# Performance work log

Measured on AMD Instinct MI355X. Metric: run time of the kernel, lower is better.

Reference implementation:

```python
import jax, jax.numpy as jnp
import numpy as np

HIDDEN_DIM = 2048
CODE_DIM = 256
CODEBOOK_SIZE = 512
FC_DIMS = [1024, 512]
BATCH = 16384
EPS = 1e-5
NEG_SLOPE = 0.01  # PyTorch LeakyReLU default


def _linear_init(key, fan_in, fan_out):
    # kaiming_uniform_(a=sqrt(3)) ~= U(-1/sqrt(fan_in), 1/sqrt(fan_in)) scaled; use uniform bound
    bound = 1.0 / np.sqrt(fan_in)
    return jax.random.uniform(key, (fan_in, fan_out), jnp.float32, -bound, bound)


def setup_inputs() -> dict:
    key = jax.random.key(0)
    ks = jax.random.split(key, 16)
    h = jax.random.normal(ks[0], (BATCH, HIDDEN_DIM), jnp.float32)
    # encoder: Linear(2048->1024, no bias), BN, LReLU, Linear(1024->512, no bias), BN, LReLU, Linear(512->256, bias)
    enc_w1 = _linear_init(ks[1], HIDDEN_DIM, FC_DIMS[0])
    enc_bn1_g = jnp.ones((FC_DIMS[0],), jnp.float32)
    enc_bn1_b = jnp.zeros((FC_DIMS[0],), jnp.float32)
    enc_w2 = _linear_init(ks[2], FC_DIMS[0], FC_DIMS[1])
    enc_bn2_g = jnp.ones((FC_DIMS[1],), jnp.float32)
    enc_bn2_b = jnp.zeros((FC_DIMS[1],), jnp.float32)
    enc_w3 = _linear_init(ks[3], FC_DIMS[1], CODE_DIM)
    enc_b3 = jax.random.uniform(ks[4], (CODE_DIM,), jnp.float32, -1/np.sqrt(FC_DIMS[1]), 1/np.sqrt(FC_DIMS[1]))
    # codebook: NearestEmbed weight shape (code_dim, codebook_size)
    codebook = jax.random.normal(ks[5], (CODE_DIM, CODEBOOK_SIZE), jnp.float32)
    # decoder: Linear(256->512, no bias), BN, LReLU, Linear(512->1024, no bias), BN, LReLU, Linear(1024->2048, bias)
    dec_w1 = _linear_init(ks[6], CODE_DIM, FC_DIMS[1])
    dec_bn1_g = jnp.ones((FC_DIMS[1],), jnp.float32)
    dec_bn1_b = jnp.zeros((FC_DIMS[1],), jnp.float32)
    dec_w2 = _linear_init(ks[7], FC_DIMS[1], FC_DIMS[0])
    dec_bn2_g = jnp.ones((FC_DIMS[0],), jnp.float32)
    dec_bn2_b = jnp.zeros((FC_DIMS[0],), jnp.float32)
    dec_w3 = _linear_init(ks[8], FC_DIMS[0], HIDDEN_DIM)
    dec_b3 = jax.random.uniform(ks[9], (HIDDEN_DIM,), jnp.float32, -1/np.sqrt(FC_DIMS[0]), 1/np.sqrt(FC_DIMS[0]))
    return dict(h=h, enc_w1=enc_w1, enc_bn1_g=enc_bn1_g, enc_bn1_b=enc_bn1_b,
                enc_w2=enc_w2, enc_bn2_g=enc_bn2_g, enc_bn2_b=enc_bn2_b,
                enc_w3=enc_w3, enc_b3=enc_b3, codebook=codebook,
                dec_w1=dec_w1, dec_bn1_g=dec_bn1_g, dec_bn1_b=dec_bn1_b,
                dec_w2=dec_w2, dec_bn2_g=dec_bn2_g, dec_bn2_b=dec_bn2_b,
                dec_w3=dec_w3, dec_b3=dec_b3)


def _bn(x, g, b):
    # BatchNorm1d, training mode: biased batch variance, eps=1e-5
    mu = jnp.mean(x, axis=0)
    var = jnp.var(x, axis=0)
    return (x - mu) * jax.lax.rsqrt(var + EPS) * g + b


def _lrelu(x):
    return jnp.where(x >= 0, x, NEG_SLOPE * x)


def _quantize(z_e, codebook):
    # nearest codebook entry; codebook is [code_dim, K]
    # dist[b,k] = ||z_e[b] - codebook[:,k]||^2 (expanded, drop constant ||z||^2 for argmin? keep full for clarity)
    d = (jnp.sum(z_e * z_e, axis=1, keepdims=True)
         - 2.0 * (z_e @ codebook)
         + jnp.sum(codebook * codebook, axis=0)[None, :])  # [B, K]
    idx = jnp.argmin(d, axis=1)  # [B]
    z_q = codebook.T[idx]        # [B, code_dim]
    return z_q, idx


def reference(h, enc_w1, enc_bn1_g, enc_bn1_b, enc_w2, enc_bn2_g, enc_bn2_b,
              enc_w3, enc_b3, codebook,
              dec_w1, dec_bn1_g, dec_bn1_b, dec_w2, dec_bn2_g, dec_bn2_b,
              dec_w3, dec_b3):
    # encoder
    x = _lrelu(_bn(h @ enc_w1, enc_bn1_g, enc_bn1_b))
    x = _lrelu(_bn(x @ enc_w2, enc_bn2_g, enc_bn2_b))
    z_e = x @ enc_w3 + enc_b3  # [B, code_dim]
    # nearest-embed quantization with straight-through estimator
    z_q_raw, code_indices = _quantize(z_e, codebook)
    z_q = z_e + jax.lax.stop_gradient(z_q_raw - z_e)
    # decoder
    y = _lrelu(_bn(z_q @ dec_w1, dec_bn1_g, dec_bn1_b))
    y = _lrelu(_bn(y @ dec_w2, dec_bn2_g, dec_bn2_b))
    h_recon = y @ dec_w3 + dec_b3  # [B, hidden_dim]
    return z_e, z_q, h_recon, code_indices
```

## Files before the change

kernel.cpp:

```cpp
#include <hip/hip_runtime.h>
#include <hip/hip_fp16.h>
#include <cstdint>
#include <cstddef>

typedef _Float16 f16;
typedef _Float16 half8 __attribute__((ext_vector_type(8)));
typedef _Float16 half4 __attribute__((ext_vector_type(4)));
typedef float floatx4 __attribute__((ext_vector_type(4)));

static constexpr size_t NB  = 16384;
static constexpr size_t DH  = 2048;
static constexpr size_t F1  = 1024;
static constexpr size_t F2  = 512;
static constexpr size_t CD  = 256;
static constexpr size_t KCB = 512;

static constexpr size_t ZE_OFF  = 0;
static constexpr size_t ZQ_OFF  = NB * CD;
static constexpr size_t HR_OFF  = 2 * NB * CD;
static constexpr size_t IDX_OFF = 2 * NB * CD + NB * DH;

static constexpr size_t O_HH   = 0;
static constexpr size_t O_HL   = O_HH + NB * DH * 2;
static constexpr size_t R1_END = O_HL + NB * DH * 2;

static constexpr size_t R_X1H = 0;
static constexpr size_t R_X1L = NB * F1 * 2;
static constexpr size_t R_X2F = 2 * NB * F1 * 2;
static constexpr size_t R_X2H = R_X2F + NB * F2 * 4;
static constexpr size_t R_X2L = R_X2H + NB * F2 * 2;
static constexpr size_t R_Y1F = 0;
static constexpr size_t R_Y1H = NB * F2 * 4;
static constexpr size_t R_Y2H = 0;

static constexpr size_t O_W1H = R1_END;
static constexpr size_t O_W1L = O_W1H + F1 * DH * 2;
static constexpr size_t O_W2H = O_W1L + F1 * DH * 2;
static constexpr size_t O_W2L = O_W2H + F2 * F1 * 2;
static constexpr size_t O_W3H = O_W2L + F2 * F1 * 2;
static constexpr size_t O_W3L = O_W3H + CD * F2 * 2;
static constexpr size_t O_CBH = O_W3L + CD * F2 * 2;
static constexpr size_t O_CBL = O_CBH + KCB * CD * 2;
static constexpr size_t O_DW1 = O_CBL + KCB * CD * 2;
static constexpr size_t O_DW2 = O_DW1 + F2 * CD * 2;
static constexpr size_t O_DW3 = O_DW2 + F1 * F2 * 2;
static constexpr size_t O_SUM = O_DW3 + DH * F1 * 2;
static constexpr size_t O_SQ  = O_SUM + 4 * 1024 * 8;
static constexpr size_t O_SC  = O_SQ + 4 * 1024 * 8;
static constexpr size_t O_SH  = O_SC + 4 * 1024 * 4;
static constexpr size_t O_CN  = O_SH + 4 * 1024 * 4;
static constexpr size_t R2    = (O_CN + 4096 + 255) & ~(size_t)255;
static constexpr size_t R2_X1F = R2;
static constexpr size_t R2_ZEH = R2;
static constexpr size_t R2_ZEL = R2 + NB * CD * 2;
static constexpr size_t R2_S   = R2 + 2 * NB * CD * 2;
static constexpr size_t R2_ZQH = R2_S + NB * KCB * 4;
static constexpr size_t R2_Y2F = R2;

#define GLLDS(src, dst)                                                          \
    __builtin_amdgcn_global_load_lds(                                            \
        (const __attribute__((address_space(1))) void*)(src),                    \
        (__attribute__((address_space(3))) void*)(dst), 16, 0, 0)

#define VMCNT(n)  asm volatile("s_waitcnt vmcnt(" #n ")" ::: "memory")

#define WAITC(n) do { switch (n) {                                               \
    case 0: asm volatile("s_waitcnt lgkmcnt(0)" ::: "memory"); break;            \
    case 1: asm volatile("s_waitcnt lgkmcnt(1)" ::: "memory"); break;            \
    case 2: asm volatile("s_waitcnt lgkmcnt(2)" ::: "memory"); break;            \
    case 3: asm volatile("s_waitcnt lgkmcnt(3)" ::: "memory"); break;            \
    case 4: asm volatile("s_waitcnt lgkmcnt(4)" ::: "memory"); break;            \
    case 5: asm volatile("s_waitcnt lgkmcnt(5)" ::: "memory"); break;            \
    case 6: asm volatile("s_waitcnt lgkmcnt(6)" ::: "memory"); break;            \
    default: asm volatile("s_waitcnt lgkmcnt(7)" ::: "memory"); break; }         \
    __builtin_amdgcn_sched_barrier(0); } while (0)

template<bool BIAS, bool STATS, bool WSPLIT>
__global__ __launch_bounds__(256)
void g3s(const f16* __restrict__ Ah_, const f16* __restrict__ Al_,
         const f16* __restrict__ Bh_, const f16* __restrict__ Bl_,
         float* __restrict__ C, const float* __restrict__ bias,
         double* __restrict__ ssum, double* __restrict__ ssq,
         f16* __restrict__ zeh, f16* __restrict__ zel,
         int M, int N, int K)
{
    __shared__ f16 lds[2][2][8192];
    const int tid  = threadIdx.x;
    const int lane = tid & 63;
    const int w    = tid >> 6;
    const int wr   = w >> 1, wn = w & 1;
    const int row0 = blockIdx.x * 128;
    const int col0 = blockIdx.y * 128;

    const int rr8 = lane >> 3;
    const int p   = (lane & 7) ^ rr8;
    const int rr  = w * 32 + rr8;
    const f16* srcH = (p < 4) ? (Ah_ + (size_t)(row0 + rr) * K + p * 8)
                              : (Bh_ + (size_t)(col0 + rr) * K + (p - 4) * 8);
    const f16* srcL = (p < 4) ? (Al_ + (size_t)(row0 + rr) * K + p * 8)
                              : (Bl_ + (size_t)(col0 + rr) * K + (p - 4) * 8);
    const int dstBase = w * 32 * 64;
    const int KT = K >> 5;

    floatx4 acc[4][4];
#pragma unroll
    for (int m = 0; m < 4; ++m)
#pragma unroll
        for (int n = 0; n < 4; ++n)
#pragma unroll
            for (int j = 0; j < 4; ++j) acc[m][n][j] = 0.f;

    const int l15 = lane & 15;
    const int sA  = lane >> 4;

    int rdA[4], rdB[4];
#pragma unroll
    for (int m = 0; m < 4; ++m) {
        const int rA = wr * 64 + m * 16 + l15;
        rdA[m] = rA * 64 + ((sA ^ (rA & 7)) << 3);
    }
#pragma unroll
    for (int n = 0; n < 4; ++n) {
        const int rB = wn * 64 + n * 16 + l15;
        rdB[n] = rB * 64 + (((4 + sA) ^ (rB & 7)) << 3);
    }

#pragma unroll
    for (int j = 0; j < 4; ++j)
        GLLDS(srcH + (size_t)j * 8 * K, &lds[0][0][dstBase + j * 512]);
#pragma unroll
    for (int j = 0; j < 4; ++j)
        GLLDS(srcL + (size_t)j * 8 * K, &lds[0][1][dstBase + j * 512]);
    VMCNT(4);
    __builtin_amdgcn_s_barrier();

    half8 afh[4], afl[4], bfh[4], bfl[4];

    for (int kt = 0; kt < KT; ++kt) {
        const int cur = kt & 1, nxt = cur ^ 1;
        const int koff = (kt + 1 < KT ? kt + 1 : kt) << 5;
        const f16* plH = lds[cur][0];
        const f16* plL = lds[cur][1];

#pragma unroll
        for (int n = 0; n < 4; ++n) bfh[n] = *(const half8*)(plH + rdB[n]);
        afh[0] = *(const half8*)(plH + rdA[0]);
        afh[1] = *(const half8*)(plH + rdA[1]);
#pragma unroll
        for (int j = 0; j < 4; ++j)
            GLLDS(srcH + (size_t)j * 8 * K + koff, &lds[nxt][0][dstBase + j * 512]);
        WAITC(1);
        __builtin_amdgcn_s_setprio(1);
#pragma unroll
        for (int m = 0; m < 4; ++m) {
            if (m + 2 < 4) afh[m + 2] = *(const half8*)(plH + rdA[m + 2]);
#pragma unroll
            for (int n = 0; n < 4; ++n)
                acc[m][n] = __builtin_amdgcn_mfma_f32_16x16x32_f16(afh[m], bfh[n], acc[m][n], 0, 0, 0);
            if (m + 1 < 4) { if (m + 2 < 4) WAITC(1); else WAITC(0); }
        }
        __builtin_amdgcn_s_setprio(0);
        VMCNT(4);
        __builtin_amdgcn_s_barrier();

#pragma unroll
        for (int n = 0; n < 4; ++n) bfl[n] = *(const half8*)(plL + rdB[n]);
        afl[0] = *(const half8*)(plL + rdA[0]);
        afl[1] = *(const half8*)(plL + rdA[1]);
#pragma unroll
        for (int j = 0; j < 4; ++j)
            GLLDS(srcL + (size_t)j * 8 * K + koff, &lds[nxt][1][dstBase + j * 512]);
        WAITC(2);
        __builtin_amdgcn_s_setprio(1);
#pragma unroll
        for (int m = 0; m < 4; ++m) {
            if (m + 2 < 4) afl[m + 2] = *(const half8*)(plL + rdA[m + 2]);
#pragma unroll
            for (int n = 0; n < 4; ++n)
                acc[m][n] = __builtin_amdgcn_mfma_f32_16x16x32_f16(afh[m], bfl[n], acc[m][n], 0, 0, 0);
        }
#pragma unroll
        for (int m = 0; m < 4; ++m) {
            WAITC(3 - m);
#pragma unroll
            for (int n = 0; n < 4; ++n)
                acc[m][n] = __builtin_amdgcn_mfma_f32_16x16x32_f16(afl[m], bfh[n], acc[m][n], 0, 0, 0);
        }
        __builtin_amdgcn_s_setprio(0);
        VMCNT(4);
        __builtin_amdgcn_s_barrier();
    }
    VMCNT(0);

    const int cb0 = col0 + wn * 64;
    const int rb0 = row0 + wr * 64 + (lane >> 4) * 4;
#pragma unroll
    for (int n = 0; n < 4; ++n) {
        const int col = cb0 + n * 16 + l15;
        const float bv = BIAS ? bias[col] : 0.f;
        double sd = 0.0, sq = 0.0;
#pragma unroll
        for (int m = 0; m < 4; ++m) {
            const int row = rb0 + m * 16;
#pragma unroll
            for (int j = 0; j < 4; ++j) {
                const float v = acc[m][n][j] + bv;
                const size_t o = (size_t)(row + j) * N + col;
                C[o] = v;
                if (WSPLIT) {
                    const f16 hv = (f16)v;
                    zeh[o] = hv;
                    zel[o] = (f16)(v - (float)hv);
                }
                if (STATS) { sd += (double)v; sq += (double)v * (double)v; }
            }
        }
        if (STATS) {
            sd += __shfl_xor(sd, 16);
            sd += __shfl_xor(sd, 32);
            sq += __shfl_xor(sq, 16);
            sq += __shfl_xor(sq, 32);
            if (lane < 16) {
                atomicAdd(ssum + col, sd);
                atomicAdd(ssq + col, sq);
            }
        }
    }
}

template<bool BIAS, bool STATS>
__global__ __launch_bounds__(256)
void g1s(const f16* __restrict__ A_, const f16* __restrict__ B_,
         float* __restrict__ C, const float* __restrict__ bias,
         double* __restrict__ ssum, double* __restrict__ ssq,
         int M, int N, int K)
{
    __shared__ f16 lds[3][8192];
    const int tid  = threadIdx.x;
    const int lane = tid & 63;
    const int w    = tid >> 6;
    const int wr   = w >> 1, wn = w & 1;
    const int row0 = blockIdx.x * 128;
    const int col0 = blockIdx.y * 128;

    const int rr8 = lane >> 3;
    const int p   = (lane & 7) ^ rr8;
    const int rr  = w * 32 + rr8;
    const f16* srcH = (p < 4) ? (A_ + (size_t)(row0 + rr) * K + p * 8)
                              : (B_ + (size_t)(col0 + rr) * K + (p - 4) * 8);
    const int dstBase = w * 32 * 64;
    const int KT = K >> 5;

    floatx4 acc[4][4];
#pragma unroll
    for (int m = 0; m < 4; ++m)
#pragma unroll
        for (int n = 0; n < 4; ++n)
#pragma unroll
            for (int j = 0; j < 4; ++j) acc[m][n][j] = 0.f;

    const int l15 = lane & 15;
    const int sA  = lane >> 4;

    int rdA[4], rdB[4];
#pragma unroll
    for (int m = 0; m < 4; ++m) {
        const int rA = wr * 64 + m * 16 + l15;
        rdA[m] = rA * 64 + ((sA ^ (rA & 7)) << 3);
    }
#pragma unroll
    for (int n = 0; n < 4; ++n) {
        const int rB = wn * 64 + n * 16 + l15;
        rdB[n] = rB * 64 + (((4 + sA) ^ (rB & 7)) << 3);
    }

#pragma unroll
    for (int j = 0; j < 4; ++j)
        GLLDS(srcH + (size_t)j * 8 * K, &lds[0][dstBase + j * 512]);
    {
        const int k1 = (KT > 1 ? 1 : 0) << 5;
#pragma unroll
        for (int j = 0; j < 4; ++j)
            GLLDS(srcH + (size_t)j * 8 * K + k1, &lds[1][dstBase + j * 512]);
    }
    VMCNT(4);
    __builtin_amdgcn_s_barrier();

    half8 afh[4], bfh[4];

    for (int kt = 0; kt < KT; ++kt) {
        const int cur = kt % 3, tgt = (kt + 2) % 3;
        const int koff = (kt + 2 < KT ? kt + 2 : KT - 1) << 5;
        const f16* plH = lds[cur];

#pragma unroll
        for (int n = 0; n < 4; ++n) bfh[n] = *(const half8*)(plH + rdB[n]);
        afh[0] = *(const half8*)(plH + rdA[0]);
        afh[1] = *(const half8*)(plH + rdA[1]);
#pragma unroll
        for (int j = 0; j < 4; ++j)
            GLLDS(srcH + (size_t)j * 8 * K + koff, &lds[tgt][dstBase + j * 512]);
        WAITC(1);
        __builtin_amdgcn_s_setprio(1);
#pragma unroll
        for (int m = 0; m < 4; ++m) {
            if (m + 2 < 4) afh[m + 2] = *(const half8*)(plH + rdA[m + 2]);
#pragma unroll
            for (int n = 0; n < 4; ++n)
                acc[m][n] = __builtin_amdgcn_mfma_f32_16x16x32_f16(afh[m], bfh[n], acc[m][n], 0, 0, 0);
            if (m + 1 < 4) { if (m + 2 < 4) WAITC(1); else WAITC(0); }
        }
        __builtin_amdgcn_s_setprio(0);
        VMCNT(4);
        __builtin_amdgcn_s_barrier();
    }
    VMCNT(0);

    const int cb0 = col0 + wn * 64;
    const int rb0 = row0 + wr * 64 + (lane >> 4) * 4;
#pragma unroll
    for (int n = 0; n < 4; ++n) {
        const int col = cb0 + n * 16 + l15;
        const float bv = BIAS ? bias[col] : 0.f;
        double sd = 0.0, sq = 0.0;
#pragma unroll
        for (int m = 0; m < 4; ++m) {
            const int row = rb0 + m * 16;
#pragma unroll
            for (int j = 0; j < 4; ++j) {
                const float v = acc[m][n][j] + bv;
                C[(size_t)(row + j) * N + col] = v;
                if (STATS) { sd += (double)v; sq += (double)v * (double)v; }
            }
        }
        if (STATS) {
            sd += __shfl_xor(sd, 16);
            sd += __shfl_xor(sd, 32);
            sq += __shfl_xor(sq, 16);
            sq += __shfl_xor(sq, 32);
            if (lane < 16) {
                atomicAdd(ssum + col, sd);
                atomicAdd(ssq + col, sq);
            }
        }
    }
}

__global__ void split_f32(const float* __restrict__ X, f16* __restrict__ hi,
                          f16* __restrict__ lo, size_t n4)
{
    const size_t stride = (size_t)gridDim.x * blockDim.x;
    for (size_t i = (size_t)blockIdx.x * blockDim.x + threadIdx.x; i < n4; i += stride) {
        const floatx4 x = ((const floatx4*)X)[i];
        half4 h, l;
#pragma unroll
        for (int j = 0; j < 4; ++j) {
            const float v = x[j];
            const f16 hv = (f16)v;
            h[j] = hv;
            l[j] = (f16)(v - (float)hv);
        }
        ((half4*)hi)[i] = h;
        ((half4*)lo)[i] = l;
    }
}

template<bool SPLIT>
__global__ void bn_apply(const float* __restrict__ X, const float* __restrict__ scale,
                         const float* __restrict__ shift, f16* __restrict__ Yhi,
                         f16* __restrict__ Ylo, size_t n4, int Nmask)
{
    const size_t stride = (size_t)gridDim.x * blockDim.x;
    for (size_t i = (size_t)blockIdx.x * blockDim.x + threadIdx.x; i < n4; i += stride) {
        const floatx4 x = ((const floatx4*)X)[i];
        const int col = (int)((i * 4) & (size_t)Nmask);
        half4 h, l;
#pragma unroll
        for (int j = 0; j < 4; ++j) {
            float v = x[j] * scale[col + j] + shift[col + j];
            v = v >= 0.f ? v : 0.01f * v;
            const f16 hv = (f16)v;
            h[j] = hv;
            if (SPLIT) l[j] = (f16)(v - (float)hv);
        }
        ((half4*)Yhi)[i] = h;
        if (SPLIT) ((half4*)Ylo)[i] = l;
    }
}

__global__ void bn_finalize(const double* __restrict__ ssum, const double* __restrict__ ssq,
                            const float* __restrict__ g, const float* __restrict__ b,
                            float* __restrict__ scale, float* __restrict__ shift, int N)
{
    const int j = blockIdx.x * blockDim.x + threadIdx.x;
    if (j < N) {
        const double inv = 1.0 / (double)NB;
        const double mean = ssum[j] * inv;
        const double var  = ssq[j] * inv - mean * mean;
        const double sc   = (double)g[j] / sqrt(var + 1e-5);
        scale[j] = (float)sc;
        shift[j] = (float)((double)b[j] - mean * sc);
    }
}

__device__ __forceinline__ void tr_body(const float* __restrict__ W, f16* __restrict__ Thi,
                                        f16* __restrict__ Tlo, int K, int N,
                                        int bx, int by, bool split)
{
    __shared__ float tile[32][33];
    const int x = threadIdx.x;
    const int y = threadIdx.y;
    const int nt = bx * 32;
    const int kt = by * 32;
#pragma unroll
    for (int i = 0; i < 32; i += 8)
        tile[y + i][x] = W[(size_t)(kt + y + i) * N + nt + x];
    __syncthreads();
#pragma unroll
    for (int i = 0; i < 32; i += 8) {
        const float v = tile[x][y + i];
        const size_t o = (size_t)(nt + y + i) * K + kt + x;
        const f16 hv = (f16)v;
        Thi[o] = hv;
        if (split) Tlo[o] = (f16)(v - (float)hv);
    }
}

__global__ void prep_weights(const float* __restrict__ ew1, const float* __restrict__ ew2,
                             const float* __restrict__ ew3, const float* __restrict__ cbk,
                             const float* __restrict__ dw1, const float* __restrict__ dw2,
                             const float* __restrict__ dw3,
                             f16* __restrict__ W1h, f16* __restrict__ W1l,
                             f16* __restrict__ W2h, f16* __restrict__ W2l,
                             f16* __restrict__ W3h, f16* __restrict__ W3l,
                             f16* __restrict__ CBh, f16* __restrict__ CBl,
                             f16* __restrict__ D1t, f16* __restrict__ D2t,
                             f16* __restrict__ D3t, float* __restrict__ cn)
{
    const int b = blockIdx.x;
    if (b < 2048)      tr_body(ew1, W1h, W1l, DH, F1, b % 32, b / 32, true);
    else if (b < 2560) { const int c = b - 2048; tr_body(ew2, W2h, W2l, F1, F2, c % 16, c / 16, true); }
    else if (b < 2688) { const int c = b - 2560; tr_body(ew3, W3h, W3l, F2, CD, c % 8,  c / 8,  true); }
    else if (b < 2816) { const int c = b - 2688; tr_body(cbk, CBh, CBl, CD, KCB, c % 16, c / 16, true); }
    else if (b < 2944) { const int c = b - 2816; tr_body(dw1, D1t, nullptr, CD, F2, c % 16, c / 16, false); }
    else if (b < 3456) { const int c = b - 2944; tr_body(dw2, D2t, nullptr, F2, F1, c % 32, c / 32, false); }
    else if (b < 5504) { const int c = b - 3456; tr_body(dw3, D3t, nullptr, F1, DH, c % 64, c / 64, false); }
    else {
        const int tid = threadIdx.y * 32 + threadIdx.x;
        const int k = (b - 5504) * 256 + tid;
        if (k < (int)KCB) {
            double s = 0.0;
            for (int d = 0; d < (int)CD; ++d) {
                const float v = cbk[(size_t)d * KCB + k];
                s += (double)v * v;
            }
            cn[k] = (float)s;
        }
    }
}

__global__ void argmin_gather(const float* __restrict__ S, const float* __restrict__ cn,
                              const float* __restrict__ cb, float* __restrict__ zq,
                              float* __restrict__ idx_out, f16* __restrict__ zqh)
{
    const int lane = threadIdx.x & 63;
    const int row  = blockIdx.x * 4 + (threadIdx.x >> 6);
    const float* Sr = S + (size_t)row * KCB;
    float best = 3.4e38f;
    int bi = 0;
#pragma unroll
    for (int i = 0; i < 8; ++i) {
        const int k = lane + 64 * i;
        const float d = cn[k] - 2.f * Sr[k];
        if (d < best) { best = d; bi = k; }
    }
#pragma unroll
    for (int off = 32; off > 0; off >>= 1) {
        const float ob = __shfl_xor(best, off);
        const int   oi = __shfl_xor(bi, off);
        if (ob < best || (ob == best && oi < bi)) { best = ob; bi = oi; }
    }
    if (lane == 0) idx_out[row] = (float)bi;
#pragma unroll
    for (int i = 0; i < 4; ++i) {
        const int d = lane + 64 * i;
        const float v = cb[(size_t)d * KCB + bi];
        zq[(size_t)row * CD + d]  = v;
        zqh[(size_t)row * CD + d] = (f16)v;
    }
}

extern "C" void kernel_launch(void* const* d_in, const int* in_sizes, int n_in,
                              void* d_out, int out_size, void* d_ws, size_t ws_size,
                              hipStream_t stream)
{
    (void)in_sizes; (void)n_in; (void)out_size; (void)ws_size;
    const float* h   = (const float*)d_in[0];
    const float* ew1 = (const float*)d_in[1];
    const float* bg1 = (const float*)d_in[2];
    const float* bb1 = (const float*)d_in[3];
    const float* ew2 = (const float*)d_in[4];
    const float* bg2 = (const float*)d_in[5];
    const float* bb2 = (const float*)d_in[6];
    const float* ew3 = (const float*)d_in[7];
    const float* eb3 = (const float*)d_in[8];
    const float* cb  = (const float*)d_in[9];
    const float* dw1 = (const float*)d_in[10];
    const float* dg1 = (const float*)d_in[11];
    const float* db1 = (const float*)d_in[12];
    const float* dw2 = (const float*)d_in[13];
    const float* dg2 = (const float*)d_in[14];
    const float* db2 = (const float*)d_in[15];
    const float* dw3 = (const float*)d_in[16];
    const float* db3 = (const float*)d_in[17];

    char* ws = (char*)d_ws;
    float* out = (float*)d_out;

    f16* Hh  = (f16*)(ws + O_HH);
    f16* Hl  = (f16*)(ws + O_HL);
    f16* W1h = (f16*)(ws + O_W1H);
    f16* W1l = (f16*)(ws + O_W1L);
    f16* W2h = (f16*)(ws + O_W2H);
    f16* W2l = (f16*)(ws + O_W2L);
    f16* W3h = (f16*)(ws + O_W3H);
    f16* W3l = (f16*)(ws + O_W3L);
    f16* CBh = (f16*)(ws + O_CBH);
    f16* CBl = (f16*)(ws + O_CBL);
    f16* D1t = (f16*)(ws + O_DW1);
    f16* D2t = (f16*)(ws + O_DW2);
    f16* D3t = (f16*)(ws + O_DW3);
    double* sum0 = (double*)(ws + O_SUM);
    double* sq0  = (double*)(ws + O_SQ);
    float* sc0 = (float*)(ws + O_SC);
    float* sh0 = (float*)(ws + O_SH);
    float* cn  = (float*)(ws + O_CN);

    float* X1f = (float*)(ws + R2_X1F);
    f16*  X1h = (f16*)(ws + R_X1H);
    f16*  X1l = (f16*)(ws + R_X1L);
    float* X2f = (float*)(ws + R_X2F);
    f16*  X2h = (f16*)(ws + R_X2H);
    f16*  X2l = (f16*)(ws + R_X2L);
    f16*  Zeh = (f16*)(ws + R2_ZEH);
    f16*  Zel = (f16*)(ws + R2_ZEL);
    float* Sb  = (float*)(ws + R2_S);
    f16*  Zqh = (f16*)(ws + R2_ZQH);
    float* Y1f = (float*)(ws + R_Y1F);
    f16*  Y1h = (f16*)(ws + R_Y1H);
    float* Y2f = (float*)(ws + R2_Y2F);
    f16*  Y2h = (f16*)(ws + R_Y2H);

    hipMemsetAsync(ws + O_SUM, 0, 4 * 1024 * 8 * 2, stream);

    split_f32<<<2048, 256, 0, stream>>>(h, Hh, Hl, NB * DH / 4);
    prep_weights<<<5506, dim3(32, 8), 0, stream>>>(ew1, ew2, ew3, cb, dw1, dw2, dw3,
        W1h, W1l, W2h, W2l, W3h, W3l, CBh, CBl, D1t, D2t, D3t, cn);

    g3s<false, true, false><<<dim3(NB / 128, F1 / 128), 256, 0, stream>>>(
        Hh, Hl, W1h, W1l, X1f, nullptr, sum0, sq0, nullptr, nullptr, NB, F1, DH);
    bn_finalize<<<4, 256, 0, stream>>>(sum0, sq0, bg1, bb1, sc0, sh0, F1);
    bn_apply<true><<<2048, 256, 0, stream>>>(X1f, sc0, sh0, X1h, X1l, NB * F1 / 4, (int)F1 - 1);

    g3s<false, true, false><<<dim3(NB / 128, F2 / 128), 256, 0, stream>>>(
        X1h, X1l, W2h, W2l, X2f, nullptr, sum0 + 1024, sq0 + 1024, nullptr, nullptr, NB, F2, F1);
    bn_finalize<<<2, 256, 0, stream>>>(sum0 + 1024, sq0 + 1024, bg2, bb2, sc0 + 1024, sh0 + 1024, F2);
    bn_apply<true><<<2048, 256, 0, stream>>>(X2f, sc0 + 1024, sh0 + 1024, X2h, X2l, NB * F2 / 4, (int)F2 - 1);

    g3s<true, false, true><<<dim3(NB / 128, CD / 128), 256, 0, stream>>>(
        X2h, X2l, W3h, W3l, out + ZE_OFF, eb3, nullptr, nullptr, Zeh, Zel, NB, CD, F2);

    g3s<false, false, false><<<dim3(NB / 128, KCB / 128), 256, 0, stream>>>(
        Zeh, Zel, CBh, CBl, Sb, nullptr, nullptr, nullptr, nullptr, nullptr, NB, KCB, CD);
    argmin_gather<<<NB / 4, 256, 0, stream>>>(Sb, cn, cb, out + ZQ_OFF, out + IDX_OFF, Zqh);

    g1s<false, true><<<dim3(NB / 128, F2 / 128), 256, 0, stream>>>(
        Zqh, D1t, Y1f, nullptr, sum0 + 2048, sq0 + 2048, NB, F2, CD);
    bn_finalize<<<2, 256, 0, stream>>>(sum0 + 2048, sq0 + 2048, dg1, db1, sc0 + 2048, sh0 + 2048, F2);
    bn_apply<false><<<2048, 256, 0, stream>>>(Y1f, sc0 + 2048, sh0 + 2048, Y1h, nullptr, NB * F2 / 4, (int)F2 - 1);

    g1s<false, true><<<dim3(NB / 128, F1 / 128), 256, 0, stream>>>(
        Y1h, D2t, Y2f, nullptr, sum0 + 3072, sq0 + 3072, NB, F1, F2);
    bn_finalize<<<4, 256, 0, stream>>>(sum0 + 3072, sq0 + 3072, dg2, db2, sc0 + 3072, sh0 + 3072, F1);
    bn_apply<false><<<2048, 256, 0, stream>>>(Y2f, sc0 + 3072, sh0 + 3072, Y2h, nullptr, NB * F1 / 4, (int)F1 - 1);

    g1s<true, false><<<dim3(NB / 128, DH / 128), 256, 0, stream>>>(
        Y2h, D3t, out + HR_OFF, db3, nullptr, nullptr, NB, DH, F1);
}
```

Measured before the change: 667.2 us.

## Enlarge GEMM tiles to 256-wide with 512 threads and 32x32x16 MFMA

```diff
diff --git a/kernel.cpp b/kernel.cpp
--- a/kernel.cpp
+++ b/kernel.cpp
@@ -7,6 +7,7 @@
 typedef _Float16 half8 __attribute__((ext_vector_type(8)));
 typedef _Float16 half4 __attribute__((ext_vector_type(4)));
 typedef float floatx4 __attribute__((ext_vector_type(4)));
+typedef float floatx16 __attribute__((ext_vector_type(16)));
 
 static constexpr size_t NB  = 16384;
 static constexpr size_t DH  = 2048;
@@ -63,66 +64,63 @@
         (__attribute__((address_space(3))) void*)(dst), 16, 0, 0)
 
 #define VMCNT(n)  asm volatile("s_waitcnt vmcnt(" #n ")" ::: "memory")
-
-#define WAITC(n) do { switch (n) {                                               \
-    case 0: asm volatile("s_waitcnt lgkmcnt(0)" ::: "memory"); break;            \
-    case 1: asm volatile("s_waitcnt lgkmcnt(1)" ::: "memory"); break;            \
-    case 2: asm volatile("s_waitcnt lgkmcnt(2)" ::: "memory"); break;            \
-    case 3: asm volatile("s_waitcnt lgkmcnt(3)" ::: "memory"); break;            \
-    case 4: asm volatile("s_waitcnt lgkmcnt(4)" ::: "memory"); break;            \
-    case 5: asm volatile("s_waitcnt lgkmcnt(5)" ::: "memory"); break;            \
-    case 6: asm volatile("s_waitcnt lgkmcnt(6)" ::: "memory"); break;            \
-    default: asm volatile("s_waitcnt lgkmcnt(7)" ::: "memory"); break; }         \
+#define LGKMCNT0 do { asm volatile("s_waitcnt lgkmcnt(0)" ::: "memory");         \
     __builtin_amdgcn_sched_barrier(0); } while (0)
 
-template<bool BIAS, bool STATS, bool WSPLIT>
-__global__ __launch_bounds__(256)
-void g3s(const f16* __restrict__ Ah_, const f16* __restrict__ Al_,
-         const f16* __restrict__ Bh_, const f16* __restrict__ Bl_,
-         float* __restrict__ C, const float* __restrict__ bias,
-         double* __restrict__ ssum, double* __restrict__ ssq,
-         f16* __restrict__ zeh, f16* __restrict__ zel,
-         int M, int N, int K)
-{
-    __shared__ f16 lds[2][2][8192];
+template<int MB, bool BIAS, bool STATS, bool WSPLIT>
+__global__ __launch_bounds__(512)
+void gemm3_w(const f16* __restrict__ Ah_, const f16* __restrict__ Al_,
+             const f16* __restrict__ Bh_, const f16* __restrict__ Bl_,
+             float* __restrict__ C, const float* __restrict__ bias,
+             double* __restrict__ ssum, double* __restrict__ ssq,
+             f16* __restrict__ zeh, f16* __restrict__ zel,
+             int M, int N, int K)
+{
+    constexpr int BM = MB * 64;
+    __shared__ f16 lds[2][2][16384];
     const int tid  = threadIdx.x;
     const int lane = tid & 63;
     const int w    = tid >> 6;
-    const int wr   = w >> 1, wn = w & 1;
-    const int row0 = blockIdx.x * 128;
-    const int col0 = blockIdx.y * 128;
+    const int wr   = w >> 2, wn = w & 3;
+    const int row0 = blockIdx.x * BM;
+    const int col0 = blockIdx.y * 256;
 
     const int rr8 = lane >> 3;
     const int p   = (lane & 7) ^ rr8;
     const int rr  = w * 32 + rr8;
-    const f16* srcH = (p < 4) ? (Ah_ + (size_t)(row0 + rr) * K + p * 8)
+    const int arr = rr & (BM - 1);
+    const f16* srcH = (p < 4) ? (Ah_ + (size_t)(row0 + arr) * K + p * 8)
                               : (Bh_ + (size_t)(col0 + rr) * K + (p - 4) * 8);
-    const f16* srcL = (p < 4) ? (Al_ + (size_t)(row0 + rr) * K + p * 8)
+    const f16* srcL = (p < 4) ? (Al_ + (size_t)(row0 + arr) * K + p * 8)
                               : (Bl_ + (size_t)(col0 + rr) * K + (p - 4) * 8);
     const int dstBase = w * 32 * 64;
     const int KT = K >> 5;
 
-    floatx4 acc[4][4];
-#pragma unroll
-    for (int m = 0; m < 4; ++m)
-#pragma unroll
-        for (int n = 0; n < 4; ++n)
-#pragma unroll
-            for (int j = 0; j < 4; ++j) acc[m][n][j] = 0.f;
-
-    const int l15 = lane & 15;
-    const int sA  = lane >> 4;
-
-    int rdA[4], rdB[4];
-#pragma unroll
-    for (int m = 0; m < 4; ++m) {
-        const int rA = wr * 64 + m * 16 + l15;
-        rdA[m] = rA * 64 + ((sA ^ (rA & 7)) << 3);
-    }
-#pragma unroll
-    for (int n = 0; n < 4; ++n) {
-        const int rB = wn * 64 + n * 16 + l15;
-        rdB[n] = rB * 64 + (((4 + sA) ^ (rB & 7)) << 3);
+    floatx16 acc[MB][2];
+#pragma unroll
+    for (int bm = 0; bm < MB; ++bm)
+#pragma unroll
+        for (int bn = 0; bn < 2; ++bn)
+#pragma unroll
+            for (int j = 0; j < 16; ++j) acc[bm][bn][j] = 0.f;
+
+    const int l31  = lane & 31;
+    const int hsel = lane >> 5;
+
+    int rdA[MB][2], rdB[2][2];
+#pragma unroll
+    for (int bm = 0; bm < MB; ++bm) {
+        const int rA = wr * (MB * 32) + bm * 32 + l31;
+#pragma unroll
+        for (int t = 0; t < 2; ++t)
+            rdA[bm][t] = rA * 64 + (((hsel + 2 * t) ^ (rA & 7)) << 3);
+    }
+#pragma unroll
+    for (int bn = 0; bn < 2; ++bn) {
+        const int rB = wn * 64 + bn * 32 + l31;
+#pragma unroll
+        for (int t = 0; t < 2; ++t)
+            rdB[bn][t] = rB * 64 + (((4 + hsel + 2 * t) ^ (rB & 7)) << 3);
     }
 
 #pragma unroll
@@ -134,7 +132,7 @@
     VMCNT(4);
     __builtin_amdgcn_s_barrier();
 
-    half8 afh[4], afl[4], bfh[4], bfl[4];
+    half8 afh[MB][2], afl[MB][2], bfh[2][2], bfl[2][2];
 
     for (int kt = 0; kt < KT; ++kt) {
         const int cur = kt & 1, nxt = cur ^ 1;
@@ -143,69 +141,79 @@
         const f16* plL = lds[cur][1];
 
 #pragma unroll
-        for (int n = 0; n < 4; ++n) bfh[n] = *(const half8*)(plH + rdB[n]);
-        afh[0] = *(const half8*)(plH + rdA[0]);
-        afh[1] = *(const half8*)(plH + rdA[1]);
+        for (int bn = 0; bn < 2; ++bn)
+#pragma unroll
+            for (int t = 0; t < 2; ++t)
+                bfh[bn][t] = *(const half8*)(plH + rdB[bn][t]);
+#pragma unroll
+        for (int bm = 0; bm < MB; ++bm)
+#pragma unroll
+            for (int t = 0; t < 2; ++t)
+                afh[bm][t] = *(const half8*)(plH + rdA[bm][t]);
 #pragma unroll
         for (int j = 0; j < 4; ++j)
             GLLDS(srcH + (size_t)j * 8 * K + koff, &lds[nxt][0][dstBase + j * 512]);
-        WAITC(1);
+        LGKMCNT0;
         __builtin_amdgcn_s_setprio(1);
 #pragma unroll
-        for (int m = 0; m < 4; ++m) {
-            if (m + 2 < 4) afh[m + 2] = *(const half8*)(plH + rdA[m + 2]);
-#pragma unroll
-            for (int n = 0; n < 4; ++n)
-                acc[m][n] = __builtin_amdgcn_mfma_f32_16x16x32_f16(afh[m], bfh[n], acc[m][n], 0, 0, 0);
-            if (m + 1 < 4) { if (m + 2 < 4) WAITC(1); else WAITC(0); }
-        }
+        for (int bm = 0; bm < MB; ++bm)
+#pragma unroll
+            for (int bn = 0; bn < 2; ++bn) {
+                acc[bm][bn] = __builtin_amdgcn_mfma_f32_32x32x16_f16(afh[bm][0], bfh[bn][0], acc[bm][bn], 0, 0, 0);
+                acc[bm][bn] = __builtin_amdgcn_mfma_f32_32x32x16_f16(afh[bm][1], bfh[bn][1], acc[bm][bn], 0, 0, 0);
+            }
         __builtin_amdgcn_s_setprio(0);
         VMCNT(4);
         __builtin_amdgcn_s_barrier();
 
 #pragma unroll
-        for (int n = 0; n < 4; ++n) bfl[n] = *(const half8*)(plL + rdB[n]);
-        afl[0] = *(const half8*)(plL + rdA[0]);
-        afl[1] = *(const half8*)(plL + rdA[1]);
+        for (int bn = 0; bn < 2; ++bn)
+#pragma unroll
+            for (int t = 0; t < 2; ++t)
+                bfl[bn][t] = *(const half8*)(plL + rdB[bn][t]);
+#pragma unroll
+        for (int bm = 0; bm < MB; ++bm)
+#pragma unroll
+            for (int t = 0; t < 2; ++t)
+                afl[bm][t] = *(const half8*)(plL + rdA[bm][t]);
 #pragma unroll
         for (int j = 0; j < 4; ++j)
             GLLDS(srcL + (size_t)j * 8 * K + koff, &lds[nxt][1][dstBase + j * 512]);
-        WAITC(2);
+        LGKMCNT0;
         __builtin_amdgcn_s_setprio(1);
 #pragma unroll
-        for (int m = 0; m < 4; ++m) {
-            if (m + 2 < 4) afl[m + 2] = *(const half8*)(plL + rdA[m + 2]);
-#pragma unroll
-            for (int n = 0; n < 4; ++n)
-                acc[m][n] = __builtin_amdgcn_mfma_f32_16x16x32_f16(afh[m], bfl[n], acc[m][n], 0, 0, 0);
-        }
-#pragma unroll
-        for (int m = 0; m < 4; ++m) {
-            WAITC(3 - m);
-#pragma unroll
-            for (int n = 0; n < 4; ++n)
-                acc[m][n] = __builtin_amdgcn_mfma_f32_16x16x32_f16(afl[m], bfh[n], acc[m][n], 0, 0, 0);
-        }
+        for (int bm = 0; bm < MB; ++bm)
+#pragma unroll
+            for (int bn = 0; bn < 2; ++bn) {
+                acc[bm][bn] = __builtin_amdgcn_mfma_f32_32x32x16_f16(afh[bm][0], bfl[bn][0], acc[bm][bn], 0, 0, 0);
+                acc[bm][bn] = __builtin_amdgcn_mfma_f32_32x32x16_f16(afh[bm][1], bfl[bn][1], acc[bm][bn], 0, 0, 0);
+            }
+#pragma unroll
+        for (int bm = 0; bm < MB; ++bm)
+#pragma unroll
+            for (int bn = 0; bn < 2; ++bn) {
+                acc[bm][bn] = __builtin_amdgcn_mfma_f32_32x32x16_f16(afl[bm][0], bfh[bn][0], acc[bm][bn], 0, 0, 0);
+                acc[bm][bn] = __builtin_amdgcn_mfma_f32_32x32x16_f16(afl[bm][1], bfh[bn][1], acc[bm][bn], 0, 0, 0);
+            }
         __builtin_amdgcn_s_setprio(0);
         VMCNT(4);
         __builtin_amdgcn_s_barrier();
     }
     VMCNT(0);
 
-    const int cb0 = col0 + wn * 64;
-    const int rb0 = row0 + wr * 64 + (lane >> 4) * 4;
-#pragma unroll
-    for (int n = 0; n < 4; ++n) {
-        const int col = cb0 + n * 16 + l15;
+#pragma unroll
+    for (int bn = 0; bn < 2; ++bn) {
+        const int col = col0 + wn * 64 + bn * 32 + l31;
         const float bv = BIAS ? bias[col] : 0.f;
         double sd = 0.0, sq = 0.0;
 #pragma unroll
-        for (int m = 0; m < 4; ++m) {
-            const int row = rb0 + m * 16;
-#pragma unroll
-            for (int j = 0; j < 4; ++j) {
-                const float v = acc[m][n][j] + bv;
-                const size_t o = (size_t)(row + j) * N + col;
+        for (int bm = 0; bm < MB; ++bm) {
+            const int rb = row0 + wr * (MB * 32) + bm * 32 + 4 * hsel;
+#pragma unroll
+            for (int r = 0; r < 16; ++r) {
+                const int row = rb + (r & 3) + 8 * (r >> 2);
+                const float v = acc[bm][bn][r] + bv;
+                const size_t o = (size_t)row * N + col;
                 C[o] = v;
                 if (WSPLIT) {
                     const f16 hv = (f16)v;
@@ -216,11 +224,9 @@
             }
         }
         if (STATS) {
-            sd += __shfl_xor(sd, 16);
             sd += __shfl_xor(sd, 32);
-            sq += __shfl_xor(sq, 16);
             sq += __shfl_xor(sq, 32);
-            if (lane < 16) {
+            if (lane < 32) {
                 atomicAdd(ssum + col, sd);
                 atomicAdd(ssq + col, sq);
             }
@@ -228,50 +234,56 @@
     }
 }
 
-template<bool BIAS, bool STATS>
-__global__ __launch_bounds__(256)
-void g1s(const f16* __restrict__ A_, const f16* __restrict__ B_,
-         float* __restrict__ C, const float* __restrict__ bias,
-         double* __restrict__ ssum, double* __restrict__ ssq,
-         int M, int N, int K)
-{
-    __shared__ f16 lds[3][8192];
+template<int MB, bool BIAS, bool STATS>
+__global__ __launch_bounds__(512)
+void gemm1_w(const f16* __restrict__ A_, const f16* __restrict__ B_,
+             float* __restrict__ C, const float* __restrict__ bias,
+             double* __restrict__ ssum, double* __restrict__ ssq,
+             int M, int N, int K)
+{
+    constexpr int BM = MB * 64;
+    __shared__ f16 lds[3][16384];
     const int tid  = threadIdx.x;
     const int lane = tid & 63;
     const int w    = tid >> 6;
-    const int wr   = w >> 1, wn = w & 1;
-    const int row0 = blockIdx.x * 128;
-    const int col0 = blockIdx.y * 128;
+    const int wr   = w >> 2, wn = w & 3;
+    const int row0 = blockIdx.x * BM;
+    const int col0 = blockIdx.y * 256;
 
     const int rr8 = lane >> 3;
     const int p   = (lane & 7) ^ rr8;
     const int rr  = w * 32 + rr8;
-    const f16* srcH = (p < 4) ? (A_ + (size_t)(row0 + rr) * K + p * 8)
+    const int arr = rr & (BM - 1);
+    const f16* srcH = (p < 4) ? (A_ + (size_t)(row0 + arr) * K + p * 8)
                               : (B_ + (size_t)(col0 + rr) * K + (p - 4) * 8);
     const int dstBase = w * 32 * 64;
     const int KT = K >> 5;
 
-    floatx4 acc[4][4];
-#pragma unroll
-    for (int m = 0; m < 4; ++m)
-#pragma unroll
-        for (int n = 0; n < 4; ++n)
-#pragma unroll
-            for (int j = 0; j < 4; ++j) acc[m][n][j] = 0.f;
-
-    const int l15 = lane & 15;
-    const int sA  = lane >> 4;
-
-    int rdA[4], rdB[4];
-#pragma unroll
-    for (int m = 0; m < 4; ++m) {
-        const int rA = wr * 64 + m * 16 + l15;
-        rdA[m] = rA * 64 + ((sA ^ (rA & 7)) << 3);
-    }
-#pragma unroll
-    for (int n = 0; n < 4; ++n) {
-        const int rB = wn * 64 + n * 16 + l15;
-        rdB[n] = rB * 64 + (((4 + sA) ^ (rB & 7)) << 3);
+    floatx16 acc[MB][2];
+#pragma unroll
+    for (int bm = 0; bm < MB; ++bm)
+#pragma unroll
+        for (int bn = 0; bn < 2; ++bn)
+#pragma unroll
+            for (int j = 0; j < 16; ++j) acc[bm][bn][j] = 0.f;
+
+    const int l31  = lane & 31;
+    const int hsel = lane >> 5;
+
+    int rdA[MB][2], rdB[2][2];
+#pragma unroll
+    for (int bm = 0; bm < MB; ++bm) {
+        const int rA = wr * (MB * 32) + bm * 32 + l31;
+#pragma unroll
+        for (int t = 0; t < 2; ++t)
+            rdA[bm][t] = rA * 64 + (((hsel + 2 * t) ^ (rA & 7)) << 3);
+    }
+#pragma unroll
+    for (int bn = 0; bn < 2; ++bn) {
+        const int rB = wn * 64 + bn * 32 + l31;
+#pragma unroll
+        for (int t = 0; t < 2; ++t)
+            rdB[bn][t] = rB * 64 + (((4 + hsel + 2 * t) ^ (rB & 7)) << 3);
     }
 
 #pragma unroll
@@ -286,7 +298,7 @@
     VMCNT(4);
     __builtin_amdgcn_s_barrier();
 
-    half8 afh[4], bfh[4];
+    half8 afh[MB][2], bfh[2][2];
 
     for (int kt = 0; kt < KT; ++kt) {
         const int cur = kt % 3, tgt = (kt + 2) % 3;
@@ -294,51 +306,53 @@
         const f16* plH = lds[cur];
 
 #pragma unroll
-        for (int n = 0; n < 4; ++n) bfh[n] = *(const half8*)(plH + rdB[n]);
-        afh[0] = *(const half8*)(plH + rdA[0]);
-        afh[1] = *(const half8*)(plH + rdA[1]);
+        for (int bn = 0; bn < 2; ++bn)
+#pragma unroll
+            for (int t = 0; t < 2; ++t)
+                bfh[bn][t] = *(const half8*)(plH + rdB[bn][t]);
+#pragma unroll
+        for (int bm = 0; bm < MB; ++bm)
+#pragma unroll
+            for (int t = 0; t < 2; ++t)
+                afh[bm][t] = *(const half8*)(plH + rdA[bm][t]);
 #pragma unroll
         for (int j = 0; j < 4; ++j)
             GLLDS(srcH + (size_t)j * 8 * K + koff, &lds[tgt][dstBase + j * 512]);
-        WAITC(1);
+        LGKMCNT0;
         __builtin_amdgcn_s_setprio(1);
 #pragma unroll
-        for (int m = 0; m < 4; ++m) {
-            if (m + 2 < 4) afh[m + 2] = *(const half8*)(plH + rdA[m + 2]);
-#pragma unroll
-            for (int n = 0; n < 4; ++n)
-                acc[m][n] = __builtin_amdgcn_mfma_f32_16x16x32_f16(afh[m], bfh[n], acc[m][n], 0, 0, 0);
-            if (m + 1 < 4) { if (m + 2 < 4) WAITC(1); else WAITC(0); }
-        }
+        for (int bm = 0; bm < MB; ++bm)
+#pragma unroll
+            for (int bn = 0; bn < 2; ++bn) {
+                acc[bm][bn] = __builtin_amdgcn_mfma_f32_32x32x16_f16(afh[bm][0], bfh[bn][0], acc[bm][bn], 0, 0, 0);
+                acc[bm][bn] = __builtin_amdgcn_mfma_f32_32x32x16_f16(afh[bm][1], bfh[bn][1], acc[bm][bn], 0, 0, 0);
+            }
         __builtin_amdgcn_s_setprio(0);
         VMCNT(4);
         __builtin_amdgcn_s_barrier();
     }
     VMCNT(0);
 
-    const int cb0 = col0 + wn * 64;
-    const int rb0 = row0 + wr * 64 + (lane >> 4) * 4;
-#pragma unroll
-    for (int n = 0; n < 4; ++n) {
-        const int col = cb0 + n * 16 + l15;
+#pragma unroll
+    for (int bn = 0; bn < 2; ++bn) {
+        const int col = col0 + wn * 64 + bn * 32 + l31;
         const float bv = BIAS ? bias[col] : 0.f;
         double sd = 0.0, sq = 0.0;
 #pragma unroll
-        for (int m = 0; m < 4; ++m) {
-            const int row = rb0 + m * 16;
-#pragma unroll
-            for (int j = 0; j < 4; ++j) {
-                const float v = acc[m][n][j] + bv;
-                C[(size_t)(row + j) * N + col] = v;
+        for (int bm = 0; bm < MB; ++bm) {
+            const int rb = row0 + wr * (MB * 32) + bm * 32 + 4 * hsel;
+#pragma unroll
+            for (int r = 0; r < 16; ++r) {
+                const int row = rb + (r & 3) + 8 * (r >> 2);
+                const float v = acc[bm][bn][r] + bv;
+                C[(size_t)row * N + col] = v;
                 if (STATS) { sd += (double)v; sq += (double)v * (double)v; }
             }
         }
         if (STATS) {
-            sd += __shfl_xor(sd, 16);
             sd += __shfl_xor(sd, 32);
-            sq += __shfl_xor(sq, 16);
             sq += __shfl_xor(sq, 32);
-            if (lane < 16) {
+            if (lane < 32) {
                 atomicAdd(ssum + col, sd);
                 atomicAdd(ssq + col, sq);
             }
@@ -557,33 +571,33 @@
     prep_weights<<<5506, dim3(32, 8), 0, stream>>>(ew1, ew2, ew3, cb, dw1, dw2, dw3,
         W1h, W1l, W2h, W2l, W3h, W3l, CBh, CBl, D1t, D2t, D3t, cn);
 
-    g3s<false, true, false><<<dim3(NB / 128, F1 / 128), 256, 0, stream>>>(
+    gemm3_w<4, false, true, false><<<dim3(NB / 256, F1 / 256), 512, 0, stream>>>(
         Hh, Hl, W1h, W1l, X1f, nullptr, sum0, sq0, nullptr, nullptr, NB, F1, DH);
     bn_finalize<<<4, 256, 0, stream>>>(sum0, sq0, bg1, bb1, sc0, sh0, F1);
     bn_apply<true><<<2048, 256, 0, stream>>>(X1f, sc0, sh0, X1h, X1l, NB * F1 / 4, (int)F1 - 1);
 
-    g3s<false, true, false><<<dim3(NB / 128, F2 / 128), 256, 0, stream>>>(
+    gemm3_w<2, false, true, false><<<dim3(NB / 128, F2 / 256), 512, 0, stream>>>(
         X1h, X1l, W2h, W2l, X2f, nullptr, sum0 + 1024, sq0 + 1024, nullptr, nullptr, NB, F2, F1);
     bn_finalize<<<2, 256, 0, stream>>>(sum0 + 1024, sq0 + 1024, bg2, bb2, sc0 + 1024, sh0 + 1024, F2);
     bn_apply<true><<<2048, 256, 0, stream>>>(X2f, sc0 + 1024, sh0 + 1024, X2h, X2l, NB * F2 / 4, (int)F2 - 1);
 
-    g3s<true, false, true><<<dim3(NB / 128, CD / 128), 256, 0, stream>>>(
+    gemm3_w<2, true, false, true><<<dim3(NB / 128, CD / 256), 512, 0, stream>>>(
         X2h, X2l, W3h, W3l, out + ZE_OFF, eb3, nullptr, nullptr, Zeh, Zel, NB, CD, F2);
 
-    g3s<false, false, false><<<dim3(NB / 128, KCB / 128), 256, 0, stream>>>(
+    gemm3_w<2, false, false, false><<<dim3(NB / 128, KCB / 256), 512, 0, stream>>>(
         Zeh, Zel, CBh, CBl, Sb, nullptr, nullptr, nullptr, nullptr, nullptr, NB, KCB, CD);
     argmin_gather<<<NB / 4, 256, 0, stream>>>(Sb, cn, cb, out + ZQ_OFF, out + IDX_OFF, Zqh);
 
-    g1s<false, true><<<dim3(NB / 128, F2 / 128), 256, 0, stream>>>(
+    gemm1_w<2, false, true><<<dim3(NB / 128, F2 / 256), 512, 0, stream>>>(
         Zqh, D1t, Y1f, nullptr, sum0 + 2048, sq0 + 2048, NB, F2, CD);
     bn_finalize<<<2, 256, 0, stream>>>(sum0 + 2048, sq0 + 2048, dg1, db1, sc0 + 2048, sh0 + 2048, F2);
     bn_apply<false><<<2048, 256, 0, stream>>>(Y1f, sc0 + 2048, sh0 + 2048, Y1h, nullptr, NB * F2 / 4, (int)F2 - 1);
 
-    g1s<false, true><<<dim3(NB / 128, F1 / 128), 256, 0, stream>>>(
+    gemm1_w<4, false, true><<<dim3(NB / 256, F1 / 256), 512, 0, stream>>>(
         Y1h, D2t, Y2f, nullptr, sum0 + 3072, sq0 + 3072, NB, F1, F2);
     bn_finalize<<<4, 256, 0, stream>>>(sum0 + 3072, sq0 + 3072, dg2, db2, sc0 + 3072, sh0 + 3072, F1);
     bn_apply<false><<<2048, 256, 0, stream>>>(Y2f, sc0 + 3072, sh0 + 3072, Y2h, nullptr, NB * F1 / 4, (int)F1 - 1);
 
-    g1s<true, false><<<dim3(NB / 128, DH / 128), 256, 0, stream>>>(
+    gemm1_w<4, true, false><<<dim3(NB / 256, DH / 256), 512, 0, stream>>>(
         Y2h, D3t, out + HR_OFF, db3, nullptr, nullptr, NB, DH, F1);
 }
```

Measured after the change: 608.2 us. 8.8% less time.
